# Kernel tuning notes

Measured on AMD Instinct MI355X. Metric: run time of the kernel, lower is better.

The kernel has to match this reference:

```python
import jax, jax.numpy as jnp
import numpy as np

N = 262144          # nodes
M = 1048576         # edges
F = 64              # elem_fea_len
HG = 128            # gate hidden
HM = 128            # message hidden
HEADS = 3
WEIGHT_POW = 1.0
NEG_SLOPE = 0.01    # LeakyReLU default


def _leaky(x):
    return jnp.where(x >= 0, x, NEG_SLOPE * x)


def setup_inputs() -> dict:
    key = jax.random.key(0)
    ks = jax.random.split(key, 12)
    s = lambda *sh: 1.0 / np.sqrt(sh[-2]) if len(sh) >= 2 else 0.0
    inp = {
        "elem_weights": jax.random.uniform(ks[0], (N, 1), dtype=jnp.float32),
        "elem_in_fea": jax.random.normal(ks[1], (N, F), dtype=jnp.float32),
        "self_fea_idx": jnp.sort(jax.random.randint(ks[2], (M,), 0, N)),
        "nbr_fea_idx": jax.random.randint(ks[3], (M,), 0, N),
        # per-head gate network: Linear(2F->HG) + LeakyReLU + Linear(HG->1)
        "gate_w1": jax.random.normal(ks[4], (HEADS, 2 * F, HG), dtype=jnp.float32) * (1.0 / np.sqrt(2 * F)),
        "gate_b1": jnp.zeros((HEADS, HG), dtype=jnp.float32),
        "gate_w2": jax.random.normal(ks[5], (HEADS, HG, 1), dtype=jnp.float32) * (1.0 / np.sqrt(HG)),
        "gate_b2": jnp.zeros((HEADS, 1), dtype=jnp.float32),
        # per-head message network: Linear(2F->HM) + LeakyReLU + Linear(HM->F)
        "msg_w1": jax.random.normal(ks[6], (HEADS, 2 * F, HM), dtype=jnp.float32) * (1.0 / np.sqrt(2 * F)),
        "msg_b1": jnp.zeros((HEADS, HM), dtype=jnp.float32),
        "msg_w2": jax.random.normal(ks[7], (HEADS, HM, F), dtype=jnp.float32) * (1.0 / np.sqrt(HM)),
        "msg_b2": jnp.zeros((HEADS, F), dtype=jnp.float32),
    }
    return inp


def reference(elem_weights, elem_in_fea, self_fea_idx, nbr_fea_idx,
              gate_w1, gate_b1, gate_w2, gate_b2,
              msg_w1, msg_b1, msg_w2, msg_b2):
    n_nodes = elem_in_fea.shape[0]
    # gather edge endpoint features: (M, 2F)
    fea = jnp.concatenate([elem_in_fea[self_fea_idx], elem_in_fea[nbr_fea_idx]], axis=1)
    w = elem_weights[nbr_fea_idx, 0]  # (M,)
    w_pow = w ** WEIGHT_POW

    head_out = []
    for h in range(gate_w1.shape[0]):
        # gate logits (M,)
        g = (_leaky(fea @ gate_w1[h] + gate_b1[h]) @ gate_w2[h] + gate_b2[h])[:, 0]
        # weighted segment softmax over edges grouped by self node
        gmax = jax.ops.segment_max(g, self_fea_idx, num_segments=n_nodes)
        e = w_pow * jnp.exp(g - gmax[self_fea_idx])
        denom = jax.ops.segment_sum(e, self_fea_idx, num_segments=n_nodes)
        attn = e / (denom[self_fea_idx] + 1e-10)  # (M,)
        # message (M, F)
        m = _leaky(fea @ msg_w1[h] + msg_b1[h]) @ msg_w2[h] + msg_b2[h]
        # scatter-add weighted messages to nodes (N, F)
        head_out.append(jax.ops.segment_sum(attn[:, None] * m, self_fea_idx, num_segments=n_nodes))

    pooled = jnp.mean(jnp.stack(head_out), axis=0)
    return pooled + elem_in_fea
```

## Files before the change

kernel.cpp:

```cpp
#include <hip/hip_runtime.h>

#define NNODE 262144
#define NEDGE 1048576
#define NTILES 8192
#define NEG 0.01f

typedef __bf16 bf16x8 __attribute__((ext_vector_type(8)));
typedef float f32x4 __attribute__((ext_vector_type(4)));
typedef unsigned short u16;
typedef u16 u16x8 __attribute__((ext_vector_type(8)));
typedef unsigned int u32;

__device__ __forceinline__ u16 f2bf(float f) {
    u32 u = __float_as_uint(f);
    u = u + 0x7FFFu + ((u >> 16) & 1u);
    return (u16)(u >> 16);
}
__device__ __forceinline__ u32 encf(float f) {
    u32 u = __float_as_uint(f);
    return (u & 0x80000000u) ? ~u : (u | 0x80000000u);
}
__device__ __forceinline__ float decf(u32 k) {
    return (k & 0x80000000u) ? __uint_as_float(k ^ 0x80000000u) : __uint_as_float(~k);
}
__device__ __forceinline__ float lrelu(float x) { return x >= 0.f ? x : NEG * x; }

__device__ __forceinline__ void lgkm_bar() {
    asm volatile("s_waitcnt lgkmcnt(0)" ::: "memory");
    __builtin_amdgcn_s_barrier();
}

template <int LD>
__device__ __forceinline__ bf16x8 load_bfrag(const float* __restrict__ p) {
    u16x8 t;
#pragma unroll
    for (int j = 0; j < 8; ++j) t[j] = f2bf(p[j * LD]);
    return __builtin_bit_cast(bf16x8, t);
}

template <bool TAB>
__global__ void k_init(const float* __restrict__ fea, float* __restrict__ out,
                       u32* __restrict__ gmaxk, float* __restrict__ denom,
                       u16* __restrict__ fea16) {
    int i = blockIdx.x * 256 + threadIdx.x;
    float4 v = ((const float4*)fea)[i];
    ((float4*)out)[i] = v;
    if (TAB) {
        ushort4 s;
        s.x = f2bf(v.x); s.y = f2bf(v.y); s.z = f2bf(v.z); s.w = f2bf(v.w);
        ((ushort4*)fea16)[i] = s;
    }
    if (i < 3 * NNODE) { gmaxk[i] = 0u; denom[i] = 0.f; }
}

template <bool TAB, int NTHR>
__device__ __forceinline__ void stage_A(u16* Al, int tile, int tid,
                                        const float* __restrict__ fea,
                                        const u16* __restrict__ fea16,
                                        const int* __restrict__ selfi,
                                        const int* __restrict__ nbri) {
    for (int idx = tid; idx < 2048; idx += NTHR) {
        int el = idx >> 4;
        int part = idx & 15;
        int edge = tile * 128 + el;
        int node = (part < 8) ? selfi[edge] : nbri[edge];
        int c8 = (part & 7) << 3;
        int col0 = ((part >> 3) << 6) + c8;
        u16x8 sv;
        if (TAB) {
            sv = *(const u16x8*)(fea16 + node * 64 + c8);
        } else {
            float4 f0 = *(const float4*)(fea + node * 64 + c8);
            float4 f1 = *(const float4*)(fea + node * 64 + c8 + 4);
            sv[0] = f2bf(f0.x); sv[1] = f2bf(f0.y); sv[2] = f2bf(f0.z); sv[3] = f2bf(f0.w);
            sv[4] = f2bf(f1.x); sv[5] = f2bf(f1.y); sv[6] = f2bf(f1.z); sv[7] = f2bf(f1.w);
        }
        *(u16x8*)(Al + el * 136 + col0) = sv;
    }
}

template <bool TAB>
__global__ __launch_bounds__(384, 3) void k_gate(
    const float* __restrict__ fea, const u16* __restrict__ fea16,
    const int* __restrict__ selfi, const int* __restrict__ nbri,
    const float* __restrict__ gw1, const float* __restrict__ gb1,
    const float* __restrict__ gw2, const float* __restrict__ gb2,
    float* __restrict__ g_out, u32* __restrict__ gmaxk) {
    __shared__ u16 Al[128 * 136];
    __shared__ float gpart[6][128];
    const int tid = threadIdx.x;
    const int w = tid >> 6, l = tid & 63, q = l >> 4, c = l & 15;
    const int hw = w >> 1;
    const int ntb = (w & 1) * 4;

    bf16x8 wf[4][4];
    {
        const float* W = gw1 + hw * 16384;
#pragma unroll
        for (int t = 0; t < 4; ++t)
#pragma unroll
            for (int kk = 0; kk < 4; ++kk)
                wf[t][kk] = load_bfrag<128>(W + (kk * 32 + q * 8) * 128 + (ntb + t) * 16 + c);
    }
    float b1v[4], w2v[4];
#pragma unroll
    for (int t = 0; t < 4; ++t) {
        b1v[t] = gb1[hw * 128 + (ntb + t) * 16 + c];
        w2v[t] = gw2[hw * 128 + (ntb + t) * 16 + c];
    }

    for (int tile = blockIdx.x; tile < NTILES; tile += gridDim.x) {
        stage_A<TAB, 384>(Al, tile, tid, fea, fea16, selfi, nbri);
        lgkm_bar();

#pragma unroll
        for (int eb = 0; eb < 8; ++eb) {
            const u16* arow = Al + (eb * 16 + c) * 136 + q * 8;
            bf16x8 a0 = *(const bf16x8*)(arow);
            bf16x8 a1 = *(const bf16x8*)(arow + 32);
            bf16x8 a2 = *(const bf16x8*)(arow + 64);
            bf16x8 a3 = *(const bf16x8*)(arow + 96);
            float gp[4] = {0.f, 0.f, 0.f, 0.f};
#pragma unroll
            for (int t = 0; t < 4; ++t) {
                f32x4 acc = {0.f, 0.f, 0.f, 0.f};
                acc = __builtin_amdgcn_mfma_f32_16x16x32_bf16(a0, wf[t][0], acc, 0, 0, 0);
                acc = __builtin_amdgcn_mfma_f32_16x16x32_bf16(a1, wf[t][1], acc, 0, 0, 0);
                acc = __builtin_amdgcn_mfma_f32_16x16x32_bf16(a2, wf[t][2], acc, 0, 0, 0);
                acc = __builtin_amdgcn_mfma_f32_16x16x32_bf16(a3, wf[t][3], acc, 0, 0, 0);
#pragma unroll
                for (int r = 0; r < 4; ++r)
                    gp[r] += lrelu(acc[r] + b1v[t]) * w2v[t];
            }
#pragma unroll
            for (int m = 1; m < 16; m <<= 1) {
#pragma unroll
                for (int r = 0; r < 4; ++r) gp[r] += __shfl_xor(gp[r], m, 64);
            }
            if (c == 0) {
#pragma unroll
                for (int r = 0; r < 4; ++r) gpart[w][eb * 16 + q * 4 + r] = gp[r];
            }
        }
        lgkm_bar();

        if (tid < 128) {
            int e = tile * 128 + tid;
            int s = selfi[e];
#pragma unroll
            for (int h = 0; h < 3; ++h) {
                float g = gpart[2 * h][tid] + gpart[2 * h + 1][tid] + gb2[h];
                g_out[h * NEDGE + e] = g;
                atomicMax(gmaxk + h * NNODE + s, encf(g));
            }
        }
    }
}

__global__ void k_denom(const float* __restrict__ ew,
                        const int* __restrict__ selfi, const int* __restrict__ nbri,
                        float* __restrict__ e_buf, const u32* __restrict__ gmaxk,
                        float* __restrict__ denom) {
    int t = blockIdx.x * 256 + threadIdx.x;
    int e0 = t * 4;
    int4 s4 = *(const int4*)(selfi + e0);
    int4 n4 = *(const int4*)(nbri + e0);
    float w0 = ew[n4.x], w1 = ew[n4.y], w2 = ew[n4.z], w3 = ew[n4.w];
#pragma unroll
    for (int h = 0; h < 3; ++h) {
        float4 g4 = *(const float4*)(e_buf + h * NEDGE + e0);
        const u32* gm = gmaxk + h * NNODE;
        float v0 = w0 * __expf(g4.x - decf(gm[s4.x]));
        float v1 = w1 * __expf(g4.y - decf(gm[s4.y]));
        float v2 = w2 * __expf(g4.z - decf(gm[s4.z]));
        float v3 = w3 * __expf(g4.w - decf(gm[s4.w]));
        float4 o = {v0, v1, v2, v3};
        *(float4*)(e_buf + h * NEDGE + e0) = o;
        float* dn = denom + h * NNODE;
        if (s4.x == s4.y) v1 += v0; else atomicAdd(dn + s4.x, v0);
        if (s4.y == s4.z) v2 += v1; else atomicAdd(dn + s4.y, v1);
        if (s4.z == s4.w) v3 += v2; else atomicAdd(dn + s4.z, v2);
        atomicAdd(dn + s4.w, v3);
    }
}

template <bool TAB>
__global__ __launch_bounds__(512, 4) void k_msg(
    const float* __restrict__ fea, const u16* __restrict__ fea16,
    const int* __restrict__ selfi, const int* __restrict__ nbri,
    const float* __restrict__ mw1, const float* __restrict__ mb1,
    const float* __restrict__ mw2, const float* __restrict__ mb2,
    const float* __restrict__ e_buf, const float* __restrict__ denom,
    float* __restrict__ out) {
    __shared__ u16 Al[128 * 136];
    __shared__ u16 Hl[128 * 136];
    __shared__ float attn_l[2][128];
    __shared__ int self_l[2][128];
    const int h = blockIdx.y;
    const int tid = threadIdx.x;
    const int w = tid >> 6, l = tid & 63, q = l >> 4, c = l & 15;
    const int eg1 = w & 1, tg = w >> 1;
    const int eg2 = w >> 1, ng = w & 1;

    bf16x8 w1f[2][4];
    {
        const float* W1 = mw1 + h * 16384;
#pragma unroll
        for (int t = 0; t < 2; ++t)
#pragma unroll
            for (int kk = 0; kk < 4; ++kk)
                w1f[t][kk] = load_bfrag<128>(W1 + (kk * 32 + q * 8) * 128 + (tg * 2 + t) * 16 + c);
    }
    bf16x8 w2f[2][4];
    {
        const float* W2 = mw2 + h * 8192;
#pragma unroll
        for (int n2 = 0; n2 < 2; ++n2)
#pragma unroll
            for (int kk = 0; kk < 4; ++kk)
                w2f[n2][kk] = load_bfrag<64>(W2 + (kk * 32 + q * 8) * 64 + (ng * 2 + n2) * 16 + c);
    }
    float4 b1q[2];
#pragma unroll
    for (int t = 0; t < 2; ++t)
        b1q[t] = *(const float4*)(mb1 + h * 128 + (tg * 2 + t) * 16 + q * 4);
    float b2v[2];
#pragma unroll
    for (int n2 = 0; n2 < 2; ++n2) b2v[n2] = mb2[h * 64 + (ng * 2 + n2) * 16 + c];

    int pb = 0;
    for (int tile = blockIdx.x; tile < NTILES; tile += gridDim.x, pb ^= 1) {
        stage_A<TAB, 512>(Al, tile, tid, fea, fea16, selfi, nbri);
        if (tid < 128) {
            int e = tile * 128 + tid;
            int s = selfi[e];
            self_l[pb][tid] = s;
            attn_l[pb][tid] = e_buf[h * NEDGE + e] / (denom[h * NNODE + s] + 1e-10f) * (1.f / 3.f);
        }
        lgkm_bar();

#pragma unroll
        for (int ebi = 0; ebi < 4; ++ebi) {
            int eb = eg1 * 4 + ebi;
            const u16* arow = Al + (eb * 16 + c) * 136 + q * 8;
            bf16x8 a0 = *(const bf16x8*)(arow);
            bf16x8 a1 = *(const bf16x8*)(arow + 32);
            bf16x8 a2 = *(const bf16x8*)(arow + 64);
            bf16x8 a3 = *(const bf16x8*)(arow + 96);
#pragma unroll
            for (int t = 0; t < 2; ++t) {
                f32x4 acc = {0.f, 0.f, 0.f, 0.f};
                acc = __builtin_amdgcn_mfma_f32_16x16x32_bf16(w1f[t][0], a0, acc, 0, 0, 0);
                acc = __builtin_amdgcn_mfma_f32_16x16x32_bf16(w1f[t][1], a1, acc, 0, 0, 0);
                acc = __builtin_amdgcn_mfma_f32_16x16x32_bf16(w1f[t][2], a2, acc, 0, 0, 0);
                acc = __builtin_amdgcn_mfma_f32_16x16x32_bf16(w1f[t][3], a3, acc, 0, 0, 0);
                ushort4 hv;
                hv.x = f2bf(lrelu(acc[0] + b1q[t].x));
                hv.y = f2bf(lrelu(acc[1] + b1q[t].y));
                hv.z = f2bf(lrelu(acc[2] + b1q[t].z));
                hv.w = f2bf(lrelu(acc[3] + b1q[t].w));
                *(ushort4*)(Hl + (eb * 16 + c) * 136 + (tg * 2 + t) * 16 + q * 4) = hv;
            }
        }
        lgkm_bar();

#pragma unroll
        for (int ebi = 0; ebi < 2; ++ebi) {
            int eb = eg2 * 2 + ebi;
            const u16* hrow = Hl + (eb * 16 + c) * 136 + q * 8;
            bf16x8 h0 = *(const bf16x8*)(hrow);
            bf16x8 h1 = *(const bf16x8*)(hrow + 32);
            bf16x8 h2 = *(const bf16x8*)(hrow + 64);
            bf16x8 h3 = *(const bf16x8*)(hrow + 96);
            int rb = eb * 16 + q * 4;
            int s0 = self_l[pb][rb], s1 = self_l[pb][rb + 1];
            int s2 = self_l[pb][rb + 2], s3 = self_l[pb][rb + 3];
            float a0 = attn_l[pb][rb], a1 = attn_l[pb][rb + 1];
            float a2v = attn_l[pb][rb + 2], a3 = attn_l[pb][rb + 3];
#pragma unroll
            for (int n2 = 0; n2 < 2; ++n2) {
                f32x4 m = {0.f, 0.f, 0.f, 0.f};
                m = __builtin_amdgcn_mfma_f32_16x16x32_bf16(h0, w2f[n2][0], m, 0, 0, 0);
                m = __builtin_amdgcn_mfma_f32_16x16x32_bf16(h1, w2f[n2][1], m, 0, 0, 0);
                m = __builtin_amdgcn_mfma_f32_16x16x32_bf16(h2, w2f[n2][2], m, 0, 0, 0);
                m = __builtin_amdgcn_mfma_f32_16x16x32_bf16(h3, w2f[n2][3], m, 0, 0, 0);
                int col = (ng * 2 + n2) * 16 + c;
                float v0 = a0 * (m[0] + b2v[n2]);
                float v1 = a1 * (m[1] + b2v[n2]);
                float v2 = a2v * (m[2] + b2v[n2]);
                float v3 = a3 * (m[3] + b2v[n2]);
                if (s0 == s1) v1 += v0; else atomicAdd(out + s0 * 64 + col, v0);
                if (s1 == s2) v2 += v1; else atomicAdd(out + s1 * 64 + col, v1);
                if (s2 == s3) v3 += v2; else atomicAdd(out + s2 * 64 + col, v2);
                atomicAdd(out + s3 * 64 + col, v3);
            }
        }
    }
}

extern "C" void kernel_launch(void* const* d_in, const int* in_sizes, int n_in,
                              void* d_out, int out_size, void* d_ws, size_t ws_size,
                              hipStream_t stream) {
    const float* ew   = (const float*)d_in[0];
    const float* fea  = (const float*)d_in[1];
    const int* selfi  = (const int*)d_in[2];
    const int* nbri   = (const int*)d_in[3];
    const float* gw1  = (const float*)d_in[4];
    const float* gb1  = (const float*)d_in[5];
    const float* gw2  = (const float*)d_in[6];
    const float* gb2  = (const float*)d_in[7];
    const float* mw1  = (const float*)d_in[8];
    const float* mb1  = (const float*)d_in[9];
    const float* mw2  = (const float*)d_in[10];
    const float* mb2  = (const float*)d_in[11];
    float* out = (float*)d_out;
    char* ws = (char*)d_ws;

    float* e_buf = (float*)ws;
    u32* gmaxk   = (u32*)(ws + 12582912);
    float* denom = (float*)(ws + 15728640);
    u16* fea16   = (u16*)(ws + 18874368);
    const bool tab = ws_size >= (size_t)52428800;

    if (tab) {
        k_init<true><<<dim3(16384), dim3(256), 0, stream>>>(fea, out, gmaxk, denom, fea16);
        k_gate<true><<<dim3(512), dim3(384), 0, stream>>>(fea, fea16, selfi, nbri,
                                                          gw1, gb1, gw2, gb2, e_buf, gmaxk);
    } else {
        k_init<false><<<dim3(16384), dim3(256), 0, stream>>>(fea, out, gmaxk, denom, fea16);
        k_gate<false><<<dim3(512), dim3(384), 0, stream>>>(fea, fea16, selfi, nbri,
                                                           gw1, gb1, gw2, gb2, e_buf, gmaxk);
    }
    k_denom<<<dim3(1024), dim3(256), 0, stream>>>(ew, selfi, nbri, e_buf, gmaxk, denom);
    if (tab) {
        k_msg<true><<<dim3(512, 3), dim3(512), 0, stream>>>(fea, fea16, selfi, nbri,
                                                            mw1, mb1, mw2, mb2, e_buf, denom, out);
    } else {
        k_msg<false><<<dim3(512, 3), dim3(512), 0, stream>>>(fea, fea16, selfi, nbri,
                                                             mw1, mb1, mw2, mb2, e_buf, denom, out);
    }
}
```

Measured before the change: 885.1 us.

## Software-pipeline edge feature gathers across tiles and swap MFMA operands in gate kernel

The per-tile gather of node features into LDS is replaced by a register-staged software pipeline in both the gate and message kernels. Indices are prefetched two tiles ahead and gathers one tile ahead, so the global gather latency overlaps the MFMA work of the current tile. The gate kernel also swaps the MFMA operand order, so each lane reduces across its accumulator rows and needs only two shuffles instead of a 16-lane butterfly. The manual bf16 rounding is replaced with the compiler's native conversion, which may map to a hardware instruction. The extra staging registers raise register pressure, which at the fixed launch bounds could cause spills or lower occupancy.

```diff
diff --git a/kernel.cpp b/kernel.cpp
--- a/kernel.cpp
+++ b/kernel.cpp
@@ -11,11 +11,7 @@
 typedef u16 u16x8 __attribute__((ext_vector_type(8)));
 typedef unsigned int u32;
 
-__device__ __forceinline__ u16 f2bf(float f) {
-    u32 u = __float_as_uint(f);
-    u = u + 0x7FFFu + ((u >> 16) & 1u);
-    return (u16)(u >> 16);
-}
+__device__ __forceinline__ u16 cvt_bf(float f) { return __builtin_bit_cast(u16, (__bf16)f); }
 __device__ __forceinline__ u32 encf(float f) {
     u32 u = __float_as_uint(f);
     return (u & 0x80000000u) ? ~u : (u | 0x80000000u);
@@ -34,7 +30,7 @@
 __device__ __forceinline__ bf16x8 load_bfrag(const float* __restrict__ p) {
     u16x8 t;
 #pragma unroll
-    for (int j = 0; j < 8; ++j) t[j] = f2bf(p[j * LD]);
+    for (int j = 0; j < 8; ++j) t[j] = cvt_bf(p[j * LD]);
     return __builtin_bit_cast(bf16x8, t);
 }
 
@@ -47,36 +43,10 @@
     ((float4*)out)[i] = v;
     if (TAB) {
         ushort4 s;
-        s.x = f2bf(v.x); s.y = f2bf(v.y); s.z = f2bf(v.z); s.w = f2bf(v.w);
+        s.x = cvt_bf(v.x); s.y = cvt_bf(v.y); s.z = cvt_bf(v.z); s.w = cvt_bf(v.w);
         ((ushort4*)fea16)[i] = s;
     }
     if (i < 3 * NNODE) { gmaxk[i] = 0u; denom[i] = 0.f; }
-}
-
-template <bool TAB, int NTHR>
-__device__ __forceinline__ void stage_A(u16* Al, int tile, int tid,
-                                        const float* __restrict__ fea,
-                                        const u16* __restrict__ fea16,
-                                        const int* __restrict__ selfi,
-                                        const int* __restrict__ nbri) {
-    for (int idx = tid; idx < 2048; idx += NTHR) {
-        int el = idx >> 4;
-        int part = idx & 15;
-        int edge = tile * 128 + el;
-        int node = (part < 8) ? selfi[edge] : nbri[edge];
-        int c8 = (part & 7) << 3;
-        int col0 = ((part >> 3) << 6) + c8;
-        u16x8 sv;
-        if (TAB) {
-            sv = *(const u16x8*)(fea16 + node * 64 + c8);
-        } else {
-            float4 f0 = *(const float4*)(fea + node * 64 + c8);
-            float4 f1 = *(const float4*)(fea + node * 64 + c8 + 4);
-            sv[0] = f2bf(f0.x); sv[1] = f2bf(f0.y); sv[2] = f2bf(f0.z); sv[3] = f2bf(f0.w);
-            sv[4] = f2bf(f1.x); sv[5] = f2bf(f1.y); sv[6] = f2bf(f1.z); sv[7] = f2bf(f1.w);
-        }
-        *(u16x8*)(Al + el * 136 + col0) = sv;
-    }
 }
 
 template <bool TAB>
@@ -102,56 +72,113 @@
             for (int kk = 0; kk < 4; ++kk)
                 wf[t][kk] = load_bfrag<128>(W + (kk * 32 + q * 8) * 128 + (ntb + t) * 16 + c);
     }
-    float b1v[4], w2v[4];
+    float4 b1q[4], w2q[4];
 #pragma unroll
     for (int t = 0; t < 4; ++t) {
-        b1v[t] = gb1[hw * 128 + (ntb + t) * 16 + c];
-        w2v[t] = gw2[hw * 128 + (ntb + t) * 16 + c];
-    }
-
-    for (int tile = blockIdx.x; tile < NTILES; tile += gridDim.x) {
-        stage_A<TAB, 384>(Al, tile, tid, fea, fea16, selfi, nbri);
+        b1q[t] = *(const float4*)(gb1 + hw * 128 + (ntb + t) * 16 + q * 4);
+        w2q[t] = *(const float4*)(gw2 + hw * 128 + (ntb + t) * 16 + q * 4);
+    }
+
+    const int part = tid & 15;
+    const int c8 = (part & 7) << 3;
+    const int colw = ((part >> 3) << 6) + c8;
+    const bool isSelf = part < 8;
+    const int el0 = tid >> 4;
+    const bool v5 = tid < 128;
+    const int STRIDE = gridDim.x;
+
+    int iv[6];
+    u16x8 gT[6]; float4 gA[6], gB[6];
+
+    auto loadIdx = [&](int tt) {
+#pragma unroll
+        for (int it = 0; it < 6; ++it) {
+            if (it < 5 || v5) {
+                int edge = tt * 128 + el0 + it * 24;
+                iv[it] = isSelf ? selfi[edge] : nbri[edge];
+            }
+        }
+    };
+    auto issueGather = [&]() {
+#pragma unroll
+        for (int it = 0; it < 6; ++it) {
+            if (it < 5 || v5) {
+                if (TAB) gT[it] = *(const u16x8*)(fea16 + (size_t)iv[it] * 64 + c8);
+                else {
+                    gA[it] = *(const float4*)(fea + (size_t)iv[it] * 64 + c8);
+                    gB[it] = *(const float4*)(fea + (size_t)iv[it] * 64 + c8 + 4);
+                }
+            }
+        }
+    };
+    auto commitStage = [&]() {
+#pragma unroll
+        for (int it = 0; it < 6; ++it) {
+            if (it < 5 || v5) {
+                u16x8 sv;
+                if (TAB) sv = gT[it];
+                else {
+#pragma unroll
+                    for (int j = 0; j < 4; ++j) { sv[j] = cvt_bf(gA[it][j]); sv[4 + j] = cvt_bf(gB[it][j]); }
+                }
+                *(u16x8*)(Al + (el0 + it * 24) * 136 + colw) = sv;
+            }
+        }
+    };
+
+    int t = blockIdx.x;
+    int sGc = 0, sGn = 0;
+    loadIdx(t);
+    if (v5) sGc = selfi[t * 128 + tid];
+    issueGather();
+    { int t1 = t + STRIDE; if (t1 >= NTILES) t1 = t;
+      loadIdx(t1);
+      if (v5) sGn = selfi[t1 * 128 + tid]; }
+
+    for (; t < NTILES; t += STRIDE) {
+        commitStage();
         lgkm_bar();
+
+        int t1 = t + STRIDE; if (t1 >= NTILES) t1 = t;
+        int t2 = t1 + STRIDE; if (t2 >= NTILES) t2 = t1;
+        issueGather();
+        loadIdx(t2);
+        int sUse = sGc; sGc = sGn;
+        if (v5) sGn = selfi[t2 * 128 + tid];
 
 #pragma unroll
         for (int eb = 0; eb < 8; ++eb) {
             const u16* arow = Al + (eb * 16 + c) * 136 + q * 8;
-            bf16x8 a0 = *(const bf16x8*)(arow);
-            bf16x8 a1 = *(const bf16x8*)(arow + 32);
-            bf16x8 a2 = *(const bf16x8*)(arow + 64);
-            bf16x8 a3 = *(const bf16x8*)(arow + 96);
-            float gp[4] = {0.f, 0.f, 0.f, 0.f};
-#pragma unroll
-            for (int t = 0; t < 4; ++t) {
+            bf16x8 e0 = *(const bf16x8*)(arow);
+            bf16x8 e1 = *(const bf16x8*)(arow + 32);
+            bf16x8 e2 = *(const bf16x8*)(arow + 64);
+            bf16x8 e3 = *(const bf16x8*)(arow + 96);
+            float gp = 0.f;
+#pragma unroll
+            for (int tt = 0; tt < 4; ++tt) {
                 f32x4 acc = {0.f, 0.f, 0.f, 0.f};
-                acc = __builtin_amdgcn_mfma_f32_16x16x32_bf16(a0, wf[t][0], acc, 0, 0, 0);
-                acc = __builtin_amdgcn_mfma_f32_16x16x32_bf16(a1, wf[t][1], acc, 0, 0, 0);
-                acc = __builtin_amdgcn_mfma_f32_16x16x32_bf16(a2, wf[t][2], acc, 0, 0, 0);
-                acc = __builtin_amdgcn_mfma_f32_16x16x32_bf16(a3, wf[t][3], acc, 0, 0, 0);
-#pragma unroll
-                for (int r = 0; r < 4; ++r)
-                    gp[r] += lrelu(acc[r] + b1v[t]) * w2v[t];
-            }
-#pragma unroll
-            for (int m = 1; m < 16; m <<= 1) {
-#pragma unroll
-                for (int r = 0; r < 4; ++r) gp[r] += __shfl_xor(gp[r], m, 64);
-            }
-            if (c == 0) {
-#pragma unroll
-                for (int r = 0; r < 4; ++r) gpart[w][eb * 16 + q * 4 + r] = gp[r];
-            }
+                acc = __builtin_amdgcn_mfma_f32_16x16x32_bf16(wf[tt][0], e0, acc, 0, 0, 0);
+                acc = __builtin_amdgcn_mfma_f32_16x16x32_bf16(wf[tt][1], e1, acc, 0, 0, 0);
+                acc = __builtin_amdgcn_mfma_f32_16x16x32_bf16(wf[tt][2], e2, acc, 0, 0, 0);
+                acc = __builtin_amdgcn_mfma_f32_16x16x32_bf16(wf[tt][3], e3, acc, 0, 0, 0);
+                gp += lrelu(acc[0] + b1q[tt].x) * w2q[tt].x;
+                gp += lrelu(acc[1] + b1q[tt].y) * w2q[tt].y;
+                gp += lrelu(acc[2] + b1q[tt].z) * w2q[tt].z;
+                gp += lrelu(acc[3] + b1q[tt].w) * w2q[tt].w;
+            }
+            gp += __shfl_xor(gp, 16, 64);
+            gp += __shfl_xor(gp, 32, 64);
+            if (q == 0) gpart[w][eb * 16 + c] = gp;
         }
         lgkm_bar();
 
         if (tid < 128) {
-            int e = tile * 128 + tid;
-            int s = selfi[e];
-#pragma unroll
-            for (int h = 0; h < 3; ++h) {
-                float g = gpart[2 * h][tid] + gpart[2 * h + 1][tid] + gb2[h];
-                g_out[h * NEDGE + e] = g;
-                atomicMax(gmaxk + h * NNODE + s, encf(g));
+            int e = t * 128 + tid;
+#pragma unroll
+            for (int hh = 0; hh < 3; ++hh) {
+                float g = gpart[2 * hh][tid] + gpart[2 * hh + 1][tid] + gb2[hh];
+                g_out[hh * NEDGE + e] = g;
+                atomicMax(gmaxk + hh * NNODE + sUse, encf(g));
             }
         }
     }
@@ -228,16 +255,73 @@
 #pragma unroll
     for (int n2 = 0; n2 < 2; ++n2) b2v[n2] = mb2[h * 64 + (ng * 2 + n2) * 16 + c];
 
+    const int part = tid & 15;
+    const int c8 = (part & 7) << 3;
+    const int colw = ((part >> 3) << 6) + c8;
+    const bool isSelf = part < 8;
+    const int el0 = tid >> 4;
+    const bool isAttn = tid < 128;
+    const int STRIDE = gridDim.x;
+
+    int iv[4];
+    u16x8 gT[4]; float4 gA[4], gB[4];
+
+    auto loadIdx = [&](int tt) {
+#pragma unroll
+        for (int it = 0; it < 4; ++it) {
+            int edge = tt * 128 + el0 + it * 32;
+            iv[it] = isSelf ? selfi[edge] : nbri[edge];
+        }
+    };
+    auto issueGather = [&]() {
+#pragma unroll
+        for (int it = 0; it < 4; ++it) {
+            if (TAB) gT[it] = *(const u16x8*)(fea16 + (size_t)iv[it] * 64 + c8);
+            else {
+                gA[it] = *(const float4*)(fea + (size_t)iv[it] * 64 + c8);
+                gB[it] = *(const float4*)(fea + (size_t)iv[it] * 64 + c8 + 4);
+            }
+        }
+    };
+    auto commitStage = [&]() {
+#pragma unroll
+        for (int it = 0; it < 4; ++it) {
+            u16x8 sv;
+            if (TAB) sv = gT[it];
+            else {
+#pragma unroll
+                for (int j = 0; j < 4; ++j) { sv[j] = cvt_bf(gA[it][j]); sv[4 + j] = cvt_bf(gB[it][j]); }
+            }
+            *(u16x8*)(Al + (el0 + it * 32) * 136 + colw) = sv;
+        }
+    };
+
+    int t = blockIdx.x;
+    float ebv = 0.f, dnv = 1.f;
+    int sAc = 0, sAn = 0;
+    loadIdx(t);
+    if (isAttn) sAc = selfi[t * 128 + tid];
+    issueGather();
+    if (isAttn) { ebv = e_buf[h * NEDGE + t * 128 + tid]; dnv = denom[h * NNODE + sAc]; }
+    { int t1 = t + STRIDE; if (t1 >= NTILES) t1 = t;
+      loadIdx(t1);
+      if (isAttn) sAn = selfi[t1 * 128 + tid]; }
+
     int pb = 0;
-    for (int tile = blockIdx.x; tile < NTILES; tile += gridDim.x, pb ^= 1) {
-        stage_A<TAB, 512>(Al, tile, tid, fea, fea16, selfi, nbri);
-        if (tid < 128) {
-            int e = tile * 128 + tid;
-            int s = selfi[e];
-            self_l[pb][tid] = s;
-            attn_l[pb][tid] = e_buf[h * NEDGE + e] / (denom[h * NNODE + s] + 1e-10f) * (1.f / 3.f);
+    for (; t < NTILES; t += STRIDE, pb ^= 1) {
+        commitStage();
+        if (isAttn) {
+            self_l[pb][tid] = sAc;
+            attn_l[pb][tid] = ebv / (dnv + 1e-10f) * (1.f / 3.f);
         }
         lgkm_bar();
+
+        int t1 = t + STRIDE; if (t1 >= NTILES) t1 = t;
+        int t2 = t1 + STRIDE; if (t2 >= NTILES) t2 = t1;
+        issueGather();
+        if (isAttn) { ebv = e_buf[h * NEDGE + t1 * 128 + tid]; dnv = denom[h * NNODE + sAn]; }
+        loadIdx(t2);
+        if (isAttn) { sAc = sAn; sAn = selfi[t2 * 128 + tid]; }
 
 #pragma unroll
         for (int ebi = 0; ebi < 4; ++ebi) {
@@ -248,18 +332,18 @@
             bf16x8 a2 = *(const bf16x8*)(arow + 64);
             bf16x8 a3 = *(const bf16x8*)(arow + 96);
 #pragma unroll
-            for (int t = 0; t < 2; ++t) {
+            for (int tt = 0; tt < 2; ++tt) {
                 f32x4 acc = {0.f, 0.f, 0.f, 0.f};
-                acc = __builtin_amdgcn_mfma_f32_16x16x32_bf16(w1f[t][0], a0, acc, 0, 0, 0);
-                acc = __builtin_amdgcn_mfma_f32_16x16x32_bf16(w1f[t][1], a1, acc, 0, 0, 0);
-                acc = __builtin_amdgcn_mfma_f32_16x16x32_bf16(w1f[t][2], a2, acc, 0, 0, 0);
-                acc = __builtin_amdgcn_mfma_f32_16x16x32_bf16(w1f[t][3], a3, acc, 0, 0, 0);
+                acc = __builtin_amdgcn_mfma_f32_16x16x32_bf16(w1f[tt][0], a0, acc, 0, 0, 0);
+                acc = __builtin_amdgcn_mfma_f32_16x16x32_bf16(w1f[tt][1], a1, acc, 0, 0, 0);
+                acc = __builtin_amdgcn_mfma_f32_16x16x32_bf16(w1f[tt][2], a2, acc, 0, 0, 0);
+                acc = __builtin_amdgcn_mfma_f32_16x16x32_bf16(w1f[tt][3], a3, acc, 0, 0, 0);
                 ushort4 hv;
-                hv.x = f2bf(lrelu(acc[0] + b1q[t].x));
-                hv.y = f2bf(lrelu(acc[1] + b1q[t].y));
-                hv.z = f2bf(lrelu(acc[2] + b1q[t].z));
-                hv.w = f2bf(lrelu(acc[3] + b1q[t].w));
-                *(ushort4*)(Hl + (eb * 16 + c) * 136 + (tg * 2 + t) * 16 + q * 4) = hv;
+                hv.x = cvt_bf(lrelu(acc[0] + b1q[tt].x));
+                hv.y = cvt_bf(lrelu(acc[1] + b1q[tt].y));
+                hv.z = cvt_bf(lrelu(acc[2] + b1q[tt].z));
+                hv.w = cvt_bf(lrelu(acc[3] + b1q[tt].w));
+                *(ushort4*)(Hl + (eb * 16 + c) * 136 + (tg * 2 + tt) * 16 + q * 4) = hv;
             }
         }
         lgkm_bar();
```

Measured after the change: 1.007 ms. 13.8% more time.
